# Kernel optimization log

Measured on AMD Instinct MI355X. Metric: run time of the kernel, lower is better.

## Reference

```python
import jax, jax.numpy as jnp
import numpy as np


def _wn(W, g):
    # weight_norm with dim=None: scalar g times W / ||W||_F
    return (g / jnp.linalg.norm(W)) * W


def setup_inputs() -> dict:
    key = jax.random.key(0)
    ks = jax.random.split(key, 8)
    B, N, D = 16, 1024, 128
    v_dim = q_dim = 1024
    K = 1024 * 3  # h_dim * k
    h_out = 8
    s = 0.02
    return {
        "v": jax.random.normal(ks[0], (B, N, v_dim), jnp.float32),
        "q": jax.random.normal(ks[1], (B, D, q_dim), jnp.float32),
        "Wv": jax.random.normal(ks[2], (K, v_dim), jnp.float32) * s,
        "gv": jnp.ones((), jnp.float32),
        "bv": jax.random.normal(ks[3], (K,), jnp.float32) * s,
        "Wq": jax.random.normal(ks[4], (K, q_dim), jnp.float32) * s,
        "gq": jnp.ones((), jnp.float32),
        "bq": jax.random.normal(ks[5], (K,), jnp.float32) * s,
        "h_mat": jax.random.normal(ks[6], (1, h_out, 1, K), jnp.float32) * s,
        "h_bias": jnp.zeros((1, h_out, 1, 1), jnp.float32),
    }


def reference(v, q, Wv, gv, bv, Wq, gq, bq, h_mat, h_bias):
    # v_net / q_net: single weight-normed Linear (dropout inactive at inference)
    v_ = jnp.einsum('bnc,kc->bnk', v, _wn(Wv, gv)) + bv  # (B,N,K)
    q_ = jnp.einsum('bdc,kc->bdk', q, _wn(Wq, gq)) + bq  # (B,D,K)
    hm = h_mat[0, :, 0, :]                               # (H,K)
    # logits[b,h,n,d] = sum_k hm[h,k] * v_[b,n,k] * q_[b,d,k]
    logits = jnp.einsum('hk,bnk,bdk->bhnd', hm, v_, q_) + h_bias
    return logits
```

## Files before the change

kernel.cpp:

```cpp
#include <hip/hip_runtime.h>
#include <hip/hip_bf16.h>
#include <math.h>

typedef unsigned short u16;
typedef unsigned int u32;

typedef __bf16 bf16x8 __attribute__((ext_vector_type(8)));
typedef float f32x4 __attribute__((ext_vector_type(4)));

union U8 { uint4 u; u16 s[8]; };

__device__ __forceinline__ float b2f(u16 x) {
    u32 y = ((u32)x) << 16;
    return __builtin_bit_cast(float, y);
}
__device__ __forceinline__ u16 f2b(float f) {
    u32 x = __builtin_bit_cast(u32, f);
    u32 r = x + 0x7fffu + ((x >> 16) & 1u);
    return (u16)(r >> 16);
}
__device__ __forceinline__ uint4 cvt8(float4 a, float4 b) {
    U8 o;
    o.s[0] = f2b(a.x); o.s[1] = f2b(a.y); o.s[2] = f2b(a.z); o.s[3] = f2b(a.w);
    o.s[4] = f2b(b.x); o.s[5] = f2b(b.y); o.s[6] = f2b(b.z); o.s[7] = f2b(b.w);
    return o.u;
}

__device__ __forceinline__ void gload16(const u16* g, const u16* l) {
    __builtin_amdgcn_global_load_lds(
        (const __attribute__((address_space(1))) void*)g,
        (__attribute__((address_space(3))) void*)l, 16, 0, 0);
}


__global__ void __launch_bounds__(64) zero_ss(float* ss) {
    if (threadIdx.x < 2) ss[threadIdx.x] = 0.f;
}

__global__ void __launch_bounds__(256) sumsq_k(const float* __restrict__ Wv,
                                               const float* __restrict__ Wq,
                                               float* __restrict__ ss, int n) {
    const float* W = (blockIdx.y == 0) ? Wv : Wq;
    float acc = 0.f;
    size_t stride = (size_t)gridDim.x * 256 * 8;
    for (size_t i = ((size_t)blockIdx.x * 256 + threadIdx.x) * 8; i < (size_t)n; i += stride) {
        float4 a = *(const float4*)(W + i);
        float4 b = *(const float4*)(W + i + 4);
        acc += a.x * a.x + a.y * a.y + a.z * a.z + a.w * a.w;
        acc += b.x * b.x + b.y * b.y + b.z * b.z + b.w * b.w;
    }
#pragma unroll
    for (int o = 32; o > 0; o >>= 1) acc += __shfl_down(acc, o, 64);
    __shared__ float red[4];
    int lane = threadIdx.x & 63, wv = threadIdx.x >> 6;
    if (lane == 0) red[wv] = acc;
    __syncthreads();
    if (threadIdx.x == 0) atomicAdd(&ss[blockIdx.y], red[0] + red[1] + red[2] + red[3]);
}

__global__ void __launch_bounds__(256) twvh_k(const float* __restrict__ Wv,
                                              const float* __restrict__ hm,
                                              u16* __restrict__ wvh) {
    __shared__ float t[32][33];
    int cx0 = blockIdx.x * 32;
    int ky0 = blockIdx.y * 32;
    int tx = threadIdx.x, ty = threadIdx.y;
#pragma unroll
    for (int j = ty; j < 32; j += 8)
        t[j][tx] = Wv[(size_t)(ky0 + j) * 1024 + cx0 + tx];
    __syncthreads();
    int k = ky0 + tx;
    float hv[8];
#pragma unroll
    for (int h = 0; h < 8; h++) hv[h] = hm[(size_t)h * 3072 + k];
#pragma unroll
    for (int j = ty; j < 32; j += 8) {
        float w = t[tx][j];
        int c = cx0 + j;
#pragma unroll
        for (int h = 0; h < 8; h++)
            wvh[(size_t)h * 3145728 + (size_t)c * 3072 + k] = f2b(hv[h] * w);
    }
}

__global__ void __launch_bounds__(256) cvt_v(const float* __restrict__ v,
                                             u16* __restrict__ vb, int n) {
    size_t stride = (size_t)gridDim.x * 256 * 8;
    for (size_t i = ((size_t)blockIdx.x * 256 + threadIdx.x) * 8; i < (size_t)n; i += stride) {
        float4 a = *(const float4*)(v + i);
        float4 b = *(const float4*)(v + i + 4);
        *(uint4*)(vb + i) = cvt8(a, b);
    }
}

__global__ void __launch_bounds__(256) const_k(const u16* __restrict__ qbuf,
                                               const float* __restrict__ bv,
                                               const float* __restrict__ hm,
                                               float* __restrict__ cb) {
    int idx = blockIdx.x * 256 + threadIdx.x;
    int b = idx >> 10, hd = idx & 1023, h = hd >> 7, d = hd & 127;
    const u16* qr = qbuf + ((size_t)b * 128 + d) * 3072;
    const float* hr = hm + (size_t)h * 3072;
    float acc = 0.f;
    for (int k = 0; k < 3072; k += 8) {
        U8 uq; uq.u = *(const uint4*)(qr + k);
        float4 h0 = *(const float4*)(hr + k);
        float4 h1 = *(const float4*)(hr + k + 4);
        float4 b0 = *(const float4*)(bv + k);
        float4 b1 = *(const float4*)(bv + k + 4);
        acc += b2f(uq.s[0]) * h0.x * b0.x + b2f(uq.s[1]) * h0.y * b0.y +
               b2f(uq.s[2]) * h0.z * b0.z + b2f(uq.s[3]) * h0.w * b0.w +
               b2f(uq.s[4]) * h1.x * b1.x + b2f(uq.s[5]) * h1.y * b1.y +
               b2f(uq.s[6]) * h1.z * b1.z + b2f(uq.s[7]) * h1.w * b1.w;
    }
    cb[idx] = acc;
}

template <int EPI, bool A_BF16>
__global__ void __launch_bounds__(256)
gemm_bt(const void* __restrict__ Ap, const u16* __restrict__ Bp, void* __restrict__ C,
        const float* __restrict__ ss, int ss_idx, const float* __restrict__ g,
        const float* __restrict__ bias, const float* __restrict__ cb,
        const float* __restrict__ hbias, int kdim, size_t abatch, size_t bbatch) {
    constexpr int BK = 32;
    __shared__ __align__(16) u16 sA[2][128 * BK];
    __shared__ __align__(16) u16 sB[2][128 * BK];

    const int tid = threadIdx.x;
    const int lane = tid & 63, wv = tid >> 6;
    const int wm = (wv & 1) * 64, wn = (wv >> 1) * 64;
    const int lr = lane & 15, quad = lane >> 4;
    const int z = blockIdx.z;
    const int arow0 = blockIdx.y * 128;
    const int bcol0 = blockIdx.x * 128;

    const size_t aoff = (size_t)z * abatch;
    const size_t boff = (size_t)z * bbatch;

    const int srow = 16 * wv + (lane >> 2);
    const int qcg  = (lane & 3) ^ ((lane >> 3) & 3);
    const int lb0  = wv * 512;
    const int lb1  = lb0 + 2048;

    const u16* gB0 = Bp + boff + (size_t)(bcol0 + srow) * kdim + qcg * 8;
    const u16* gB1 = gB0 + (size_t)64 * kdim;

    const int r0 = tid >> 2, c0 = (tid & 3) * 8;
    const int w0 = r0 * 32 + (((tid & 3) ^ ((tid >> 3) & 3)) * 8);
    const int w1 = w0 + 2048;

    const u16* gA0 = nullptr; const u16* gA1 = nullptr;
    const float* fA0 = nullptr; const float* fA1 = nullptr;
    if constexpr (A_BF16) {
        gA0 = (const u16*)Ap + aoff + (size_t)(arow0 + srow) * kdim + qcg * 8;
        gA1 = gA0 + (size_t)64 * kdim;
    } else {
        fA0 = (const float*)Ap + aoff + (size_t)(arow0 + r0) * kdim + c0;
        fA1 = fA0 + (size_t)64 * kdim;
    }

    const int rsw = (quad ^ ((lr >> 1) & 3)) * 8;

    if constexpr (A_BF16) {
        gload16(gA0, sA[0] + lb0);
        gload16(gA1, sA[0] + lb1);
        gA0 += BK; gA1 += BK;
    } else {
        float4 x0 = *(const float4*)fA0, x1 = *(const float4*)(fA0 + 4);
        float4 y0 = *(const float4*)fA1, y1 = *(const float4*)(fA1 + 4);
        *(uint4*)(sA[0] + w0) = cvt8(x0, x1);
        *(uint4*)(sA[0] + w1) = cvt8(y0, y1);
        fA0 += BK; fA1 += BK;
    }
    gload16(gB0, sB[0] + lb0);
    gload16(gB1, sB[0] + lb1);
    gB0 += BK; gB1 += BK;

    f32x4 acc[4][4];
#pragma unroll
    for (int im = 0; im < 4; im++)
#pragma unroll
        for (int in = 0; in < 4; in++) acc[im][in] = (f32x4){0.f, 0.f, 0.f, 0.f};

    __syncthreads();

    int p = 0;
    for (int kt = 0; kt < kdim; kt += BK) {
        const bool more = (kt + BK < kdim);

        float4 ax0, ax1, ay0, ay1;
        if (more) {
            if constexpr (A_BF16) {
                gload16(gA0, sA[p ^ 1] + lb0);
                gload16(gA1, sA[p ^ 1] + lb1);
                gA0 += BK; gA1 += BK;
            } else {
                ax0 = *(const float4*)fA0; ax1 = *(const float4*)(fA0 + 4);
                ay0 = *(const float4*)fA1; ay1 = *(const float4*)(fA1 + 4);
                fA0 += BK; fA1 += BK;
            }
            gload16(gB0, sB[p ^ 1] + lb0);
            gload16(gB1, sB[p ^ 1] + lb1);
            gB0 += BK; gB1 += BK;
        }

        const u16* sAp = sA[p];
        const u16* sBp = sB[p];
        bf16x8 af[4], bfr[4];
#pragma unroll
        for (int im = 0; im < 4; im++)
            af[im] = *(const bf16x8*)(sAp + (wm + im * 16 + lr) * 32 + rsw);
#pragma unroll
        for (int in = 0; in < 4; in++)
            bfr[in] = *(const bf16x8*)(sBp + (wn + in * 16 + lr) * 32 + rsw);
#pragma unroll
        for (int im = 0; im < 4; im++)
#pragma unroll
            for (int in = 0; in < 4; in++)
                acc[im][in] = __builtin_amdgcn_mfma_f32_16x16x32_bf16(af[im], bfr[in], acc[im][in], 0, 0, 0);

        if (more) {
            if constexpr (!A_BF16) {
                u16* dA = sA[p ^ 1];
                *(uint4*)(dA + w0) = cvt8(ax0, ax1);
                *(uint4*)(dA + w1) = cvt8(ay0, ay1);
            }
        }
        __syncthreads();
        p ^= 1;
    }

    float scale = 1.f;
    if constexpr (EPI == 0 || EPI == 2) scale = g[0] / sqrtf(ss[ss_idx]);

#pragma unroll
    for (int im = 0; im < 4; im++) {
#pragma unroll
        for (int in = 0; in < 4; in++) {
#pragma unroll
            for (int reg = 0; reg < 4; reg++) {
                int gr = arow0 + wm + im * 16 + quad * 4 + reg;
                int gc = bcol0 + wn + in * 16 + lr;
                float val = acc[im][in][reg];
                if constexpr (EPI == 0) {
                    ((u16*)C)[(size_t)gr * 3072 + gc] = f2b(val * scale + bias[gc]);
                } else if constexpr (EPI == 1) {
                    size_t idx = (((size_t)(gr >> 7) * 8 + (gc >> 10)) * 128 + (gr & 127)) * 1024
                               + (gc & 1023);
                    ((u16*)C)[idx] = f2b(val);
                } else {
                    int h = gc >> 7, d = gc & 127;
                    float o = val * scale + cb[(size_t)z * 1024 + gc] + hbias[h];
                    ((float*)C)[(((size_t)z * 8 + h) * 1024 + gr) * 128 + d] = o;
                }
            }
        }
    }
}

template <int EPI>
__global__ void __launch_bounds__(512, 2)
gemm8p(const u16* __restrict__ Ap, const u16* __restrict__ Bp, void* __restrict__ C,
       const float* __restrict__ ss, const float* __restrict__ g,
       const float* __restrict__ cb, const float* __restrict__ hbias,
       int kdim, size_t abatch, size_t bbatch) {
    __shared__ __align__(16) u16 sAb[2][256 * 64];
    __shared__ __align__(16) u16 sBb[2][256 * 64];

    const int tid = threadIdx.x;
    const int lane = tid & 63, wv = tid >> 6;
    const int wm = (wv & 1) * 128;
    const int wn = (wv >> 1) * 64;
    const int lr = lane & 15, quad = lane >> 4;
    const int z = blockIdx.z;

    int bx, by;
    if constexpr (EPI == 1) {
        int orig = blockIdx.y * 32 + blockIdx.x;
        int xcd = orig & 7, idx = orig >> 3;
        bx = (xcd << 2) | (idx & 3);
        by = idx >> 2;
    } else {
        bx = blockIdx.x; by = blockIdx.y;
    }
    const int arow0 = by * 256, bcol0 = bx * 256;

    const size_t aoff = (size_t)z * abatch, boff = (size_t)z * bbatch;

    const int sg = (tid & 7) ^ ((tid >> 3) & 7);
    const u16* gA = Ap + aoff + (size_t)(arow0 + (tid >> 3)) * kdim + sg * 8;
    const u16* gB = Bp + boff + (size_t)(bcol0 + (tid >> 3)) * kdim + sg * 8;
    const size_t ldk64 = (size_t)64 * kdim;
    const int ldst = wv * 512;

    const int slot = (quad ^ (lane & 7)) * 8;
    const int rbA = (wm + lr) * 64 + slot;
    const int rbB = (wn + lr) * 64 + slot;

    f32x4 acc[8][4];
#pragma unroll
    for (int im = 0; im < 8; im++)
#pragma unroll
        for (int in = 0; in < 4; in++) acc[im][in] = (f32x4){0.f, 0.f, 0.f, 0.f};

    const u16* sAd = sAb[0];
    const u16* sBd = sBb[0];
    u16* dA = (u16*)sAb[1];
    u16* dB = (u16*)sBb[1];

    gload16(gB + 0 * ldk64, sBb[0] + 0 * 4096 + ldst);
    gload16(gB + 1 * ldk64, sBb[0] + 1 * 4096 + ldst);
    gload16(gB + 2 * ldk64, sBb[0] + 2 * 4096 + ldst);
    gload16(gB + 3 * ldk64, sBb[0] + 3 * 4096 + ldst);
    gload16(gA + 0 * ldk64, sAb[0] + 0 * 4096 + ldst);
    gload16(gA + 2 * ldk64, sAb[0] + 2 * 4096 + ldst);
    gload16(gA + 1 * ldk64, sAb[0] + 1 * 4096 + ldst);
    gload16(gA + 3 * ldk64, sAb[0] + 3 * 4096 + ldst);
    gA += 64; gB += 64;
    asm volatile("s_waitcnt vmcnt(0)" ::: "memory");
    __builtin_amdgcn_s_barrier();

    bf16x8 af0[4], af1[4], bf0[4], bf1[4];
#pragma unroll
    for (int n = 0; n < 4; n++) bf0[n] = *(const bf16x8*)(sBd + rbB + n * 1024);
#pragma unroll
    for (int j = 0; j < 4; j++) af0[j] = *(const bf16x8*)(sAd + rbA + j * 1024);

    const int NT = kdim >> 6;
    for (int t = 0; t < NT; ++t) {
        const bool stg = (t + 1 < NT);

#pragma unroll
        for (int j = 0; j < 4; j++) af1[j] = *(const bf16x8*)(sAd + rbA + (4 + j) * 1024);
        if (stg) {
            gload16(gB + 0 * ldk64, dB + 0 * 4096 + ldst);
            gload16(gB + 1 * ldk64, dB + 1 * 4096 + ldst);
            gload16(gB + 2 * ldk64, dB + 2 * 4096 + ldst);
            gload16(gB + 3 * ldk64, dB + 3 * 4096 + ldst);
        }
        __builtin_amdgcn_s_barrier();
        __builtin_amdgcn_s_setprio(1);
#pragma unroll
        for (int j = 0; j < 4; j++)
#pragma unroll
            for (int n = 0; n < 4; n++)
                acc[j][n] = __builtin_amdgcn_mfma_f32_16x16x32_bf16(af0[j], bf0[n], acc[j][n], 0, 0, 0);
        __builtin_amdgcn_s_setprio(0);
        __builtin_amdgcn_s_barrier();

#pragma unroll
        for (int n = 0; n < 4; n++) bf1[n] = *(const bf16x8*)(sBd + (rbB ^ 32) + n * 1024);
#pragma unroll
        for (int j = 0; j < 4; j++) af0[j] = *(const bf16x8*)(sAd + (rbA ^ 32) + j * 1024);
        if (stg) {
            gload16(gA + 0 * ldk64, dA + 0 * 4096 + ldst);
            gload16(gA + 2 * ldk64, dA + 2 * 4096 + ldst);
            gload16(gA + 1 * ldk64, dA + 1 * 4096 + ldst);
            gload16(gA + 3 * ldk64, dA + 3 * 4096 + ldst);
        }
        __builtin_amdgcn_s_barrier();
        __builtin_amdgcn_s_setprio(1);
#pragma unroll
        for (int j = 0; j < 4; j++)
#pragma unroll
            for (int n = 0; n < 4; n++)
                acc[4 + j][n] = __builtin_amdgcn_mfma_f32_16x16x32_bf16(af1[j], bf0[n], acc[4 + j][n], 0, 0, 0);
        __builtin_amdgcn_s_setprio(0);
        __builtin_amdgcn_s_barrier();

#pragma unroll
        for (int j = 0; j < 4; j++) af1[j] = *(const bf16x8*)(sAd + (rbA ^ 32) + (4 + j) * 1024);
        __builtin_amdgcn_s_barrier();
        __builtin_amdgcn_s_setprio(1);
#pragma unroll
        for (int j = 0; j < 4; j++)
#pragma unroll
            for (int n = 0; n < 4; n++)
                acc[j][n] = __builtin_amdgcn_mfma_f32_16x16x32_bf16(af0[j], bf1[n], acc[j][n], 0, 0, 0);
        __builtin_amdgcn_s_setprio(0);
        asm volatile("s_waitcnt vmcnt(2)" ::: "memory");
        __builtin_amdgcn_s_barrier();

        if (stg) {
#pragma unroll
            for (int n = 0; n < 4; n++) bf0[n] = *(const bf16x8*)(dB + rbB + n * 1024);
#pragma unroll
            for (int j = 0; j < 4; j++) af0[j] = *(const bf16x8*)(dA + rbA + j * 1024);
        }
        __builtin_amdgcn_s_barrier();
        __builtin_amdgcn_s_setprio(1);
#pragma unroll
        for (int j = 0; j < 4; j++)
#pragma unroll
            for (int n = 0; n < 4; n++)
                acc[4 + j][n] = __builtin_amdgcn_mfma_f32_16x16x32_bf16(af1[j], bf1[n], acc[4 + j][n], 0, 0, 0);
        __builtin_amdgcn_s_setprio(0);
        asm volatile("s_waitcnt vmcnt(0)" ::: "memory");
        __builtin_amdgcn_s_barrier();

        const u16* tp = sAd; sAd = dA; dA = (u16*)tp;
        tp = sBd; sBd = dB; dB = (u16*)tp;
        gA += 64; gB += 64;
    }

    float scale = 1.f;
    if constexpr (EPI == 2) scale = g[0] / sqrtf(ss[0]);

#pragma unroll
    for (int im = 0; im < 8; im++) {
#pragma unroll
        for (int in = 0; in < 4; in++) {
#pragma unroll
            for (int reg = 0; reg < 4; reg++) {
                int gr = arow0 + wm + im * 16 + quad * 4 + reg;
                int gc = bcol0 + wn + in * 16 + lr;
                float val = acc[im][in][reg];
                if constexpr (EPI == 1) {
                    size_t idx = (((size_t)(gr >> 7) * 8 + (gc >> 10)) * 128 + (gr & 127)) * 1024
                               + (gc & 1023);
                    ((u16*)C)[idx] = f2b(val);
                } else {
                    int h = gc >> 7, d = gc & 127;
                    float o = val * scale + cb[(size_t)z * 1024 + gc] + hbias[h];
                    ((float*)C)[(((size_t)z * 8 + h) * 1024 + gr) * 128 + d] = o;
                }
            }
        }
    }
}


extern "C" void kernel_launch(void* const* d_in, const int* in_sizes, int n_in,
                              void* d_out, int out_size, void* d_ws, size_t ws_size,
                              hipStream_t stream) {
    (void)in_sizes; (void)n_in; (void)out_size;
    const float* v  = (const float*)d_in[0];
    const float* q  = (const float*)d_in[1];
    const float* Wv = (const float*)d_in[2];
    const float* gv = (const float*)d_in[3];
    const float* bv = (const float*)d_in[4];
    const float* Wq = (const float*)d_in[5];
    const float* gq = (const float*)d_in[6];
    const float* bq = (const float*)d_in[7];
    const float* hm = (const float*)d_in[8];
    const float* hb = (const float*)d_in[9];
    float* out = (float*)d_out;

    char* ws = (char*)d_ws;
    float* ss   = (float*)ws;
    float* cb   = (float*)(ws + 256);
    u16*   qbuf = (u16*)(ws + 256 + 65536);
    u16*   tbuf = (u16*)(ws + 256 + 65536 + 12582912);
    u16*   vb   = (u16*)(ws + 256 + 65536 + 12582912 + 33554432);
    const size_t need_vb = 256 + 65536 + 12582912 + 33554432 + 33554432;
    const bool fullfat = (ws_size >= need_vb);

    u16* wvh = (u16*)d_out;
    u16* qb  = (u16*)((char*)d_out + 50331648);
    u16* wqb = (u16*)((char*)d_out + 54525952);

    zero_ss<<<1, 64, 0, stream>>>(ss);
    sumsq_k<<<dim3(256, 2), 256, 0, stream>>>(Wv, Wq, ss, 3072 * 1024);

    twvh_k<<<dim3(32, 96), dim3(32, 8), 0, stream>>>(Wv, hm, wvh);

    cvt_v<<<1024, 256, 0, stream>>>(q, qb, 2097152);
    cvt_v<<<1536, 256, 0, stream>>>(Wq, wqb, 3145728);

    gemm_bt<0, true><<<dim3(24, 16, 1), 256, 0, stream>>>(
        qb, wqb, qbuf, ss, 1, gq, bq, nullptr, nullptr, 1024, 0, 0);

    const_k<<<64, 256, 0, stream>>>(qbuf, bv, hm, cb);

    gemm8p<1><<<dim3(32, 8, 1), 512, 0, stream>>>(
        qbuf, wvh, tbuf, nullptr, nullptr, nullptr, nullptr, 3072, 0, 0);

    if (fullfat) {
        cvt_v<<<4096, 256, 0, stream>>>(v, vb, 16777216);
        gemm8p<2><<<dim3(4, 4, 16), 512, 0, stream>>>(
            vb, tbuf, out, ss, gv, cb, hb, 1024, 1048576, 1048576);
    } else {
        gemm_bt<2, false><<<dim3(8, 8, 16), 256, 0, stream>>>(
            v, tbuf, out, ss, 0, gv, nullptr, cb, hb, 1024, 1048576, 1048576);
    }
}
```

Measured before the change: 403.8 us.

## Cut per-iteration barriers to one and issue all global prefetches up front

Restructures the double-buffered GEMM main loop: all eight A/B global-to-LDS loads for the next tile are issued at the start of the iteration, and the eight workgroup barriers per K-step are reduced to a single barrier before reading the next buffer. Fragment registers are split into separate arrays so LDS reads for the next MFMA stage overlap the current stage. This aims to remove barrier stalls and lengthen the prefetch window, at the cost of more live fragment registers and looser inter-wave scheduling. There is a risk of a hazard: the next iteration's prefetch writes the buffer just read, guarded only by the barrier before the final MFMA stage.

Measured after the change: 392.0 us. -2.9%, faster.

```diff
diff --git a/kernel.cpp b/kernel.cpp
--- a/kernel.cpp
+++ b/kernel.cpp
@@ -303,100 +303,93 @@
 #pragma unroll
         for (int in = 0; in < 4; in++) acc[im][in] = (f32x4){0.f, 0.f, 0.f, 0.f};
 
-    const u16* sAd = sAb[0];
-    const u16* sBd = sBb[0];
-    u16* dA = (u16*)sAb[1];
-    u16* dB = (u16*)sBb[1];
-
     gload16(gB + 0 * ldk64, sBb[0] + 0 * 4096 + ldst);
     gload16(gB + 1 * ldk64, sBb[0] + 1 * 4096 + ldst);
     gload16(gB + 2 * ldk64, sBb[0] + 2 * 4096 + ldst);
     gload16(gB + 3 * ldk64, sBb[0] + 3 * 4096 + ldst);
     gload16(gA + 0 * ldk64, sAb[0] + 0 * 4096 + ldst);
+    gload16(gA + 1 * ldk64, sAb[0] + 1 * 4096 + ldst);
     gload16(gA + 2 * ldk64, sAb[0] + 2 * 4096 + ldst);
-    gload16(gA + 1 * ldk64, sAb[0] + 1 * 4096 + ldst);
     gload16(gA + 3 * ldk64, sAb[0] + 3 * 4096 + ldst);
     gA += 64; gB += 64;
     asm volatile("s_waitcnt vmcnt(0)" ::: "memory");
     __builtin_amdgcn_s_barrier();
 
-    bf16x8 af0[4], af1[4], bf0[4], bf1[4];
-#pragma unroll
-    for (int n = 0; n < 4; n++) bf0[n] = *(const bf16x8*)(sBd + rbB + n * 1024);
-#pragma unroll
-    for (int j = 0; j < 4; j++) af0[j] = *(const bf16x8*)(sAd + rbA + j * 1024);
+    const u16* sAd = sAb[0];
+    const u16* sBd = sBb[0];
+    u16* dA = (u16*)sAb[1];
+    u16* dB = (u16*)sBb[1];
+
+    bf16x8 af[4], bfr[4], af1[4], af2[4], bf2[4], af3[4];
+#pragma unroll
+    for (int n = 0; n < 4; n++) bfr[n] = *(const bf16x8*)(sBd + rbB + n * 1024);
+#pragma unroll
+    for (int j = 0; j < 4; j++) af[j] = *(const bf16x8*)(sAd + rbA + j * 1024);
 
     const int NT = kdim >> 6;
     for (int t = 0; t < NT; ++t) {
         const bool stg = (t + 1 < NT);
 
-#pragma unroll
-        for (int j = 0; j < 4; j++) af1[j] = *(const bf16x8*)(sAd + rbA + (4 + j) * 1024);
         if (stg) {
             gload16(gB + 0 * ldk64, dB + 0 * 4096 + ldst);
             gload16(gB + 1 * ldk64, dB + 1 * 4096 + ldst);
             gload16(gB + 2 * ldk64, dB + 2 * 4096 + ldst);
             gload16(gB + 3 * ldk64, dB + 3 * 4096 + ldst);
-        }
+            gload16(gA + 0 * ldk64, dA + 0 * 4096 + ldst);
+            gload16(gA + 1 * ldk64, dA + 1 * 4096 + ldst);
+            gload16(gA + 2 * ldk64, dA + 2 * 4096 + ldst);
+            gload16(gA + 3 * ldk64, dA + 3 * 4096 + ldst);
+        }
+
+#pragma unroll
+        for (int j = 0; j < 4; j++) af1[j] = *(const bf16x8*)(sAd + rbA + (4 + j) * 1024);
+        __builtin_amdgcn_s_setprio(1);
+#pragma unroll
+        for (int j = 0; j < 4; j++)
+#pragma unroll
+            for (int n = 0; n < 4; n++)
+                acc[j][n] = __builtin_amdgcn_mfma_f32_16x16x32_bf16(af[j], bfr[n], acc[j][n], 0, 0, 0);
+        __builtin_amdgcn_s_setprio(0);
+
+#pragma unroll
+        for (int n = 0; n < 4; n++) bf2[n] = *(const bf16x8*)(sBd + (rbB ^ 32) + n * 1024);
+#pragma unroll
+        for (int j = 0; j < 4; j++) af2[j] = *(const bf16x8*)(sAd + (rbA ^ 32) + j * 1024);
+        __builtin_amdgcn_s_setprio(1);
+#pragma unroll
+        for (int j = 0; j < 4; j++)
+#pragma unroll
+            for (int n = 0; n < 4; n++)
+                acc[4 + j][n] = __builtin_amdgcn_mfma_f32_16x16x32_bf16(af1[j], bfr[n], acc[4 + j][n], 0, 0, 0);
+        __builtin_amdgcn_s_setprio(0);
+
+#pragma unroll
+        for (int j = 0; j < 4; j++) af3[j] = *(const bf16x8*)(sAd + (rbA ^ 32) + (4 + j) * 1024);
+        __builtin_amdgcn_s_setprio(1);
+#pragma unroll
+        for (int j = 0; j < 4; j++)
+#pragma unroll
+            for (int n = 0; n < 4; n++)
+                acc[j][n] = __builtin_amdgcn_mfma_f32_16x16x32_bf16(af2[j], bf2[n], acc[j][n], 0, 0, 0);
+        __builtin_amdgcn_s_setprio(0);
+
+        asm volatile("s_waitcnt vmcnt(0)" ::: "memory");
+        asm volatile("s_waitcnt lgkmcnt(0)" ::: "memory");
         __builtin_amdgcn_s_barrier();
+
+        if (stg) {
+#pragma unroll
+            for (int n = 0; n < 4; n++) bfr[n] = *(const bf16x8*)(dB + rbB + n * 1024);
+#pragma unroll
+            for (int j = 0; j < 4; j++) af[j] = *(const bf16x8*)(dA + rbA + j * 1024);
+        }
         __builtin_amdgcn_s_setprio(1);
 #pragma unroll
         for (int j = 0; j < 4; j++)
 #pragma unroll
             for (int n = 0; n < 4; n++)
-                acc[j][n] = __builtin_amdgcn_mfma_f32_16x16x32_bf16(af0[j], bf0[n], acc[j][n], 0, 0, 0);
+                acc[4 + j][n] = __builtin_amdgcn_mfma_f32_16x16x32_bf16(af3[j], bf2[n], acc[4 + j][n], 0, 0, 0);
         __builtin_amdgcn_s_setprio(0);
-        __builtin_amdgcn_s_barrier();
-
-#pragma unroll
-        for (int n = 0; n < 4; n++) bf1[n] = *(const bf16x8*)(sBd + (rbB ^ 32) + n * 1024);
-#pragma unroll
-        for (int j = 0; j < 4; j++) af0[j] = *(const bf16x8*)(sAd + (rbA ^ 32) + j * 1024);
-        if (stg) {
-            gload16(gA + 0 * ldk64, dA + 0 * 4096 + ldst);
-            gload16(gA + 2 * ldk64, dA + 2 * 4096 + ldst);
-            gload16(gA + 1 * ldk64, dA + 1 * 4096 + ldst);
-            gload16(gA + 3 * ldk64, dA + 3 * 4096 + ldst);
-        }
-        __builtin_amdgcn_s_barrier();
-        __builtin_amdgcn_s_setprio(1);
-#pragma unroll
-        for (int j = 0; j < 4; j++)
-#pragma unroll
-            for (int n = 0; n < 4; n++)
-                acc[4 + j][n] = __builtin_amdgcn_mfma_f32_16x16x32_bf16(af1[j], bf0[n], acc[4 + j][n], 0, 0, 0);
-        __builtin_amdgcn_s_setprio(0);
-        __builtin_amdgcn_s_barrier();
-
-#pragma unroll
-        for (int j = 0; j < 4; j++) af1[j] = *(const bf16x8*)(sAd + (rbA ^ 32) + (4 + j) * 1024);
-        __builtin_amdgcn_s_barrier();
-        __builtin_amdgcn_s_setprio(1);
-#pragma unroll
-        for (int j = 0; j < 4; j++)
-#pragma unroll
-            for (int n = 0; n < 4; n++)
-                acc[j][n] = __builtin_amdgcn_mfma_f32_16x16x32_bf16(af0[j], bf1[n], acc[j][n], 0, 0, 0);
-        __builtin_amdgcn_s_setprio(0);
-        asm volatile("s_waitcnt vmcnt(2)" ::: "memory");
-        __builtin_amdgcn_s_barrier();
-
-        if (stg) {
-#pragma unroll
-            for (int n = 0; n < 4; n++) bf0[n] = *(const bf16x8*)(dB + rbB + n * 1024);
-#pragma unroll
-            for (int j = 0; j < 4; j++) af0[j] = *(const bf16x8*)(dA + rbA + j * 1024);
-        }
-        __builtin_amdgcn_s_barrier();
-        __builtin_amdgcn_s_setprio(1);
-#pragma unroll
-        for (int j = 0; j < 4; j++)
-#pragma unroll
-            for (int n = 0; n < 4; n++)
-                acc[4 + j][n] = __builtin_amdgcn_mfma_f32_16x16x32_bf16(af1[j], bf1[n], acc[4 + j][n], 0, 0, 0);
-        __builtin_amdgcn_s_setprio(0);
-        asm volatile("s_waitcnt vmcnt(0)" ::: "memory");
-        __builtin_amdgcn_s_barrier();
 
         const u16* tp = sAd; sAd = dA; dA = (u16*)tp;
         tp = sBd; sBd = dB; dB = (u16*)tp;
```
